# Kernel tuning notes

Measured on AMD Instinct MI355X. Metric: run time of the kernel, lower is better.

The kernel has to match this reference:

```python
import jax, jax.numpy as jnp
import numpy as np


def setup_inputs() -> dict:
    key = jax.random.key(0)
    k1, k2, k3 = jax.random.split(key, 3)
    B, K, IN, OUT = 4096, 8, 1024, 1024
    x = jax.random.normal(k1, (B, IN), dtype=jnp.float32)
    blend_weights = jax.random.uniform(k2, (B, K), dtype=jnp.float32)
    weight = jax.random.normal(k3, (K, OUT, IN), dtype=jnp.float32) * 0.01
    bias = jnp.zeros((K, OUT), dtype=jnp.float32)
    return {"x": x, "blend_weights": blend_weights, "weight": weight, "bias": bias}


def reference(x, blend_weights, weight, bias):
    # Mathematically identical to blending weights first then matvec:
    #   einsum('bk,koi->boi') then bmm  ==  per-expert GEMM then blend.
    # per-expert outputs: (b, k, o)
    expert_out = jnp.einsum('bi,koi->bko', x, weight)
    out = jnp.einsum('bk,bko->bo', blend_weights, expert_out)
    out = out + blend_weights @ bias  # (b,k) @ (k,o) -> (b,o)
    return out
```

## Files before the change

kernel.cpp:

```cpp
#include <hip/hip_runtime.h>
#include <hip/hip_bf16.h>
#include <stdint.h>

typedef short short8 __attribute__((ext_vector_type(8)));
typedef float f32x4  __attribute__((ext_vector_type(4)));
typedef unsigned short u16;

#define B_ROWS 4096
#define NEXP   8
#define IN_D   1024
#define OUT_D  1024

#define BM 128
#define BN 128
#define BK 64

__device__ __forceinline__ u16 f2bf(float f) {
    uint32_t u = __float_as_uint(f);
    uint32_t r = (u + 0x7fffu + ((u >> 16) & 1u)) >> 16;
    return (u16)r;
}

#define W_CVT_BLOCKS 8192
__global__ __launch_bounds__(256) void prep(const float* __restrict__ x,
                                            const float* __restrict__ bwt,
                                            const float* __restrict__ wgt,
                                            u16* __restrict__ ab,
                                            u16* __restrict__ wb) {
    const int bid = blockIdx.x;
    if (bid < W_CVT_BLOCKS) {
        const int i = bid * 256 + threadIdx.x;
        float4 v = reinterpret_cast<const float4*>(wgt)[i];
        ushort4 o;
        o.x = f2bf(v.x); o.y = f2bf(v.y); o.z = f2bf(v.z); o.w = f2bf(v.w);
        reinterpret_cast<ushort4*>(wb)[i] = o;
    } else {
        const int b = bid - W_CVT_BLOCKS;
        const int i4 = threadIdx.x;
        float4 v = reinterpret_cast<const float4*>(x)[(size_t)b * 256 + i4];
        float4 w0 = reinterpret_cast<const float4*>(bwt)[b * 2];
        float4 w1 = reinterpret_cast<const float4*>(bwt)[b * 2 + 1];
        float wk[8] = {w0.x, w0.y, w0.z, w0.w, w1.x, w1.y, w1.z, w1.w};
        #pragma unroll
        for (int k = 0; k < NEXP; ++k) {
            ushort4 o;
            o.x = f2bf(wk[k] * v.x); o.y = f2bf(wk[k] * v.y);
            o.z = f2bf(wk[k] * v.z); o.w = f2bf(wk[k] * v.w);
            reinterpret_cast<ushort4*>(ab)[((size_t)k * B_ROWS + b) * 256 + i4] = o;
        }
    }
}

__device__ __forceinline__ void glds16(const u16* g, u16* lds_base, int off_bytes) {
    auto gp = (const __attribute__((address_space(1))) void*)(uintptr_t)(g);
    auto lp = (__attribute__((address_space(3))) void*)(uintptr_t)((const char*)lds_base + off_bytes);
    __builtin_amdgcn_global_load_lds(gp, lp, 16, 0, 0);
}

__global__ __launch_bounds__(256) void moe_gemm(
    const u16* __restrict__ Ab,
    const u16* __restrict__ Wb,
    float* __restrict__ parts,
    float* __restrict__ out,
    int epb, int nz)
{
    __shared__ __align__(16) u16 As[BM * BK];
    __shared__ __align__(16) u16 Bs[BN * BK];

    const int nwg = gridDim.x;
    const int cpx = nwg >> 3;
    const int id  = blockIdx.x;
    const int swz = (id & 7) * cpx + (id >> 3);
    const int bz  = swz >> 8;
    const int rem = swz & 255;
    const int bm  = (rem >> 3) * BM;
    const int bn  = (rem & 7) * BN;

    const int tid  = threadIdx.x;
    const int lane = tid & 63, wid = tid >> 6;
    const int wm = wid >> 1, wn = wid & 1;
    const int lr = lane & 15, lg = lane >> 4;

    int st_row[4], st_col[4], st_off[4];
    #pragma unroll
    for (int r = 0; r < 4; ++r) {
        int c = r * 256 + wid * 64 + lane;
        st_row[r] = c >> 3;
        st_col[r] = (c & 7) * 8;
        st_off[r] = (r * 256 + wid * 64) * 16;
    }

    f32x4 acc[4][4];
    #pragma unroll
    for (int mi = 0; mi < 4; ++mi)
        #pragma unroll
        for (int ni = 0; ni < 4; ++ni)
            acc[mi][ni] = (f32x4){0.f, 0.f, 0.f, 0.f};

    const int nsteps = IN_D / BK;
    for (int e = 0; e < epb; ++e) {
        const int kexp = bz * epb + e;
        const u16* Ak = Ab + (size_t)kexp * B_ROWS * IN_D;
        const u16* Wk = Wb + (size_t)kexp * OUT_D * IN_D;

        for (int it = 0; it < nsteps; ++it) {
            const int i0 = it * BK;
            __syncthreads();
            #pragma unroll
            for (int r = 0; r < 4; ++r) {
                glds16(Ak + (size_t)(bm + st_row[r]) * IN_D + i0 + st_col[r], As, st_off[r]);
                glds16(Wk + (size_t)(bn + st_row[r]) * IN_D + i0 + st_col[r], Bs, st_off[r]);
            }
            __syncthreads();

            #pragma unroll
            for (int ks = 0; ks < 2; ++ks) {
                short8 a[4], b[4];
                #pragma unroll
                for (int mi = 0; mi < 4; ++mi)
                    a[mi] = *(const short8*)(As + (wm * 64 + mi * 16 + lr) * BK + ks * 32 + lg * 8);
                #pragma unroll
                for (int ni = 0; ni < 4; ++ni)
                    b[ni] = *(const short8*)(Bs + (wn * 64 + ni * 16 + lr) * BK + ks * 32 + lg * 8);
                #pragma unroll
                for (int mi = 0; mi < 4; ++mi)
                    #pragma unroll
                    for (int ni = 0; ni < 4; ++ni)
                        acc[mi][ni] = __builtin_amdgcn_mfma_f32_16x16x32_bf16(
                            a[mi], b[ni], acc[mi][ni], 0, 0, 0);
            }
        }
    }

    float* op = (bz == nz - 1) ? out : parts + (size_t)bz * B_ROWS * OUT_D;
    #pragma unroll
    for (int mi = 0; mi < 4; ++mi)
        #pragma unroll
        for (int ni = 0; ni < 4; ++ni)
            #pragma unroll
            for (int r = 0; r < 4; ++r) {
                const int grow = bm + wm * 64 + mi * 16 + lg * 4 + r;
                const int gcol = bn + wn * 64 + ni * 16 + lr;
                op[(size_t)grow * OUT_D + gcol] = acc[mi][ni][r];
            }
}

__global__ __launch_bounds__(256) void reduce_bias(
    const float* __restrict__ parts, const float* __restrict__ bwt,
    const float* __restrict__ bias, float* __restrict__ out, int np)
{
    const int i4 = blockIdx.x * 256 + threadIdx.x;
    const size_t total = (size_t)B_ROWS * OUT_D;
    const size_t base = (size_t)i4 * 4;
    if (base >= total) return;
    const int brow = (int)(base >> 10);
    const int o = (int)(base & 1023);

    float4 s = *reinterpret_cast<const float4*>(out + base);
    for (int z = 0; z < np; ++z) {
        float4 p = *reinterpret_cast<const float4*>(parts + (size_t)z * total + base);
        s.x += p.x; s.y += p.y; s.z += p.z; s.w += p.w;
    }
    #pragma unroll
    for (int k = 0; k < NEXP; ++k) {
        const float w = bwt[brow * NEXP + k];
        float4 bb = *reinterpret_cast<const float4*>(bias + k * OUT_D + o);
        s.x += w * bb.x; s.y += w * bb.y; s.z += w * bb.z; s.w += w * bb.w;
    }
    *reinterpret_cast<float4*>(out + base) = s;
}

__global__ __launch_bounds__(256) void naive_moe(
    const float* __restrict__ x, const float* __restrict__ bwt,
    const float* __restrict__ wgt, const float* __restrict__ bias,
    float* __restrict__ out)
{
    __shared__ float xs[IN_D];
    const int brow = blockIdx.x;
    const int o = blockIdx.y * 256 + threadIdx.x;
    for (int i = threadIdx.x; i < IN_D; i += 256) xs[i] = x[(size_t)brow * IN_D + i];
    __syncthreads();
    float acc = 0.f;
    for (int k = 0; k < NEXP; ++k) {
        const float* wr = wgt + ((size_t)k * OUT_D + o) * IN_D;
        float d = 0.f;
        for (int i = 0; i < IN_D; ++i) d += xs[i] * wr[i];
        acc += bwt[brow * NEXP + k] * (d + bias[k * OUT_D + o]);
    }
    out[(size_t)brow * OUT_D + o] = acc;
}

extern "C" void kernel_launch(void* const* d_in, const int* in_sizes, int n_in,
                              void* d_out, int out_size, void* d_ws, size_t ws_size,
                              hipStream_t stream) {
    const float* x    = (const float*)d_in[0];
    const float* bwt  = (const float*)d_in[1];
    const float* wgt  = (const float*)d_in[2];
    const float* bias = (const float*)d_in[3];
    float* out = (float*)d_out;

    const size_t a_bytes    = (size_t)NEXP * B_ROWS * IN_D * 2;
    const size_t w_bytes    = (size_t)NEXP * OUT_D * IN_D * 2;
    const size_t part_bytes = (size_t)B_ROWS * OUT_D * 4;

    if (ws_size < a_bytes + w_bytes) {
        naive_moe<<<dim3(B_ROWS, OUT_D / 256), 256, 0, stream>>>(x, bwt, wgt, bias, out);
        return;
    }

    int nz = 1;
    if      (ws_size >= a_bytes + w_bytes + 3 * part_bytes) nz = 4;
    else if (ws_size >= a_bytes + w_bytes + 1 * part_bytes) nz = 2;

    u16* ab = (u16*)d_ws;
    u16* wb = (u16*)((char*)d_ws + a_bytes);
    float* parts = (float*)((char*)d_ws + a_bytes + w_bytes);

    prep<<<W_CVT_BLOCKS + B_ROWS, 256, 0, stream>>>(x, bwt, wgt, ab, wb);

    moe_gemm<<<256 * nz, 256, 0, stream>>>(ab, wb, parts, out, NEXP / nz, nz);

    reduce_bias<<<(B_ROWS * OUT_D / 4 + 255) / 256, 256, 0, stream>>>(
        parts, bwt, bias, out, nz - 1);
}
```

Before: 211.6 us.

## Rewrite MoE GEMM as 256x256 8-wave pipelined kernel with swizzled LDS

```diff
diff --git a/kernel.cpp b/kernel.cpp
--- a/kernel.cpp
+++ b/kernel.cpp
@@ -10,10 +10,6 @@
 #define NEXP   8
 #define IN_D   1024
 #define OUT_D  1024
-
-#define BM 128
-#define BN 128
-#define BK 64
 
 __device__ __forceinline__ u16 f2bf(float f) {
     uint32_t u = __float_as_uint(f);
@@ -51,97 +47,137 @@
     }
 }
 
-__device__ __forceinline__ void glds16(const u16* g, u16* lds_base, int off_bytes) {
+__device__ __forceinline__ void glds16(const u16* g, u16* lds_base, uint32_t off) {
     auto gp = (const __attribute__((address_space(1))) void*)(uintptr_t)(g);
-    auto lp = (__attribute__((address_space(3))) void*)(uintptr_t)((const char*)lds_base + off_bytes);
+    auto lp = (__attribute__((address_space(3))) void*)(uintptr_t)((const char*)lds_base + off);
     __builtin_amdgcn_global_load_lds(gp, lp, 16, 0, 0);
 }
 
-__global__ __launch_bounds__(256) void moe_gemm(
+#define PHASE(BUF, QM, QN, LOADA, STAGE_STMT)                                     \
+  {                                                                               \
+    asm volatile("s_waitcnt vmcnt(6)" ::: "memory");                              \
+    if (LOADA) {                                                                  \
+      _Pragma("unroll") for (int mi = 0; mi < 4; ++mi)                            \
+        _Pragma("unroll") for (int ks = 0; ks < 2; ++ks)                          \
+          af[mi][ks] = *(const short8*)(ldsc + (BUF)*65536 + (QM)*16384 +         \
+                                        aRowB + mi*2048 + cXor[ks]);              \
+    }                                                                             \
+    _Pragma("unroll") for (int ni = 0; ni < 2; ++ni)                              \
+      _Pragma("unroll") for (int ks = 0; ks < 2; ++ks)                            \
+        bf[ni][ks] = *(const short8*)(ldsc + (BUF)*65536 + 32768 + (QN)*16384 +   \
+                                      bRowB + ni*2048 + cXor[ks]);                \
+    STAGE_STMT;                                                                   \
+    __builtin_amdgcn_s_barrier();                                                 \
+    __builtin_amdgcn_s_setprio(1);                                                \
+    _Pragma("unroll") for (int mi = 0; mi < 4; ++mi)                              \
+      _Pragma("unroll") for (int ni = 0; ni < 2; ++ni) {                          \
+        acc[QM][QN][mi][ni] = __builtin_amdgcn_mfma_f32_16x16x32_bf16(            \
+            af[mi][0], bf[ni][0], acc[QM][QN][mi][ni], 0, 0, 0);                  \
+        acc[QM][QN][mi][ni] = __builtin_amdgcn_mfma_f32_16x16x32_bf16(            \
+            af[mi][1], bf[ni][1], acc[QM][QN][mi][ni], 0, 0, 0);                  \
+      }                                                                           \
+    __builtin_amdgcn_s_setprio(0);                                                \
+    __builtin_amdgcn_s_barrier();                                                 \
+  }
+
+__global__ __launch_bounds__(512, 2) void moe_gemm8(
     const u16* __restrict__ Ab,
     const u16* __restrict__ Wb,
     float* __restrict__ parts,
     float* __restrict__ out,
     int epb, int nz)
 {
-    __shared__ __align__(16) u16 As[BM * BK];
-    __shared__ __align__(16) u16 Bs[BN * BK];
+    __shared__ __align__(16) u16 lds[65536];
 
     const int nwg = gridDim.x;
     const int cpx = nwg >> 3;
     const int id  = blockIdx.x;
     const int swz = (id & 7) * cpx + (id >> 3);
-    const int bz  = swz >> 8;
-    const int rem = swz & 255;
-    const int bm  = (rem >> 3) * BM;
-    const int bn  = (rem & 7) * BN;
+    const int bz  = swz >> 6;
+    const int rem = swz & 63;
+    const int bm_g = (rem >> 2) * 256;
+    const int bn_g = (rem & 3) * 256;
 
     const int tid  = threadIdx.x;
     const int lane = tid & 63, wid = tid >> 6;
-    const int wm = wid >> 1, wn = wid & 1;
+    const int wm = wid >> 2, wn = wid & 3;
     const int lr = lane & 15, lg = lane >> 4;
 
-    int st_row[4], st_col[4], st_off[4];
+    const int nt   = epb << 4;
+    const int ntm1 = nt - 1;
+    const int nit  = nt >> 1;
+
+    const int row0   = wid * 8 + (lane >> 3);
+    const int colOff = ((lane & 7) ^ (lane >> 3)) * 8;
+
+    const char* ldsc = (const char*)lds;
+    const int aRowB = (wm * 64 + lr) * 128;
+    const int bRowB = (wn * 32 + lr) * 128;
+    int cXor[2];
+    cXor[0] = (lg * 16) ^ ((lr & 7) << 4);
+    cXor[1] = (64 + lg * 16) ^ ((lr & 7) << 4);
+
+    auto STAGE = [&](int t, int isB, int h, int buf) {
+        const int kexp = bz * epb + (t >> 4);
+        const int i0 = (t & 15) << 6;
+        const u16* gp = isB
+            ? Wb + ((size_t)kexp * OUT_D + bn_g + h * 128 + row0) * IN_D + i0 + colOff
+            : Ab + ((size_t)kexp * B_ROWS + bm_g + h * 128 + row0) * IN_D + i0 + colOff;
+        const uint32_t l0 = (uint32_t)((buf << 16) + (isB << 15) + (h << 14) + (wid << 10));
+        glds16(gp, lds, l0);
+        glds16(gp + (size_t)64 * IN_D, lds, l0 + 8192);
+    };
+
+    f32x4 acc[2][2][4][2];
     #pragma unroll
-    for (int r = 0; r < 4; ++r) {
-        int c = r * 256 + wid * 64 + lane;
-        st_row[r] = c >> 3;
-        st_col[r] = (c & 7) * 8;
-        st_off[r] = (r * 256 + wid * 64) * 16;
-    }
-
-    f32x4 acc[4][4];
+    for (int a = 0; a < 2; ++a)
+      #pragma unroll
+      for (int b = 0; b < 2; ++b)
+        #pragma unroll
+        for (int c = 0; c < 4; ++c)
+          #pragma unroll
+          for (int d = 0; d < 2; ++d)
+            acc[a][b][c][d] = (f32x4){0.f, 0.f, 0.f, 0.f};
+
+    short8 af[4][2], bf[2][2];
+
+    STAGE(0, 0, 0, 0);
+    STAGE(0, 1, 0, 0);
+    STAGE(0, 1, 1, 0);
+    STAGE(0, 0, 1, 0);
+    STAGE(1, 0, 0, 1);
+    STAGE(1, 1, 0, 1);
+    asm volatile("s_waitcnt vmcnt(0)" ::: "memory");
+    __builtin_amdgcn_s_barrier();
+
+    for (int m = 0; m < nit; ++m) {
+        const int t1 = 2 * m + 1;
+        const int t2 = (t1 + 1) & ntm1;
+        const int t3 = (t1 + 2) & ntm1;
+        PHASE(0, 0, 0, 1, STAGE(t1, 1, 1, 1));
+        PHASE(0, 0, 1, 0, STAGE(t1, 0, 1, 1));
+        PHASE(0, 1, 0, 1, STAGE(t2, 0, 0, 0));
+        PHASE(0, 1, 1, 0, STAGE(t2, 1, 0, 0));
+        PHASE(1, 0, 0, 1, STAGE(t2, 1, 1, 0));
+        PHASE(1, 0, 1, 0, STAGE(t2, 0, 1, 0));
+        PHASE(1, 1, 0, 1, STAGE(t3, 0, 0, 1));
+        PHASE(1, 1, 1, 0, STAGE(t3, 1, 0, 1));
+    }
+
+    float* op = (bz == nz - 1) ? out : parts + (size_t)bz * B_ROWS * OUT_D;
     #pragma unroll
-    for (int mi = 0; mi < 4; ++mi)
+    for (int qm = 0; qm < 2; ++qm)
+      #pragma unroll
+      for (int mi = 0; mi < 4; ++mi)
         #pragma unroll
-        for (int ni = 0; ni < 4; ++ni)
-            acc[mi][ni] = (f32x4){0.f, 0.f, 0.f, 0.f};
-
-    const int nsteps = IN_D / BK;
-    for (int e = 0; e < epb; ++e) {
-        const int kexp = bz * epb + e;
-        const u16* Ak = Ab + (size_t)kexp * B_ROWS * IN_D;
-        const u16* Wk = Wb + (size_t)kexp * OUT_D * IN_D;
-
-        for (int it = 0; it < nsteps; ++it) {
-            const int i0 = it * BK;
-            __syncthreads();
+        for (int qn = 0; qn < 2; ++qn)
+          #pragma unroll
+          for (int ni = 0; ni < 2; ++ni)
             #pragma unroll
             for (int r = 0; r < 4; ++r) {
-                glds16(Ak + (size_t)(bm + st_row[r]) * IN_D + i0 + st_col[r], As, st_off[r]);
-                glds16(Wk + (size_t)(bn + st_row[r]) * IN_D + i0 + st_col[r], Bs, st_off[r]);
-            }
-            __syncthreads();
-
-            #pragma unroll
-            for (int ks = 0; ks < 2; ++ks) {
-                short8 a[4], b[4];
-                #pragma unroll
-                for (int mi = 0; mi < 4; ++mi)
-                    a[mi] = *(const short8*)(As + (wm * 64 + mi * 16 + lr) * BK + ks * 32 + lg * 8);
-                #pragma unroll
-                for (int ni = 0; ni < 4; ++ni)
-                    b[ni] = *(const short8*)(Bs + (wn * 64 + ni * 16 + lr) * BK + ks * 32 + lg * 8);
-                #pragma unroll
-                for (int mi = 0; mi < 4; ++mi)
-                    #pragma unroll
-                    for (int ni = 0; ni < 4; ++ni)
-                        acc[mi][ni] = __builtin_amdgcn_mfma_f32_16x16x32_bf16(
-                            a[mi], b[ni], acc[mi][ni], 0, 0, 0);
-            }
-        }
-    }
-
-    float* op = (bz == nz - 1) ? out : parts + (size_t)bz * B_ROWS * OUT_D;
-    #pragma unroll
-    for (int mi = 0; mi < 4; ++mi)
-        #pragma unroll
-        for (int ni = 0; ni < 4; ++ni)
-            #pragma unroll
-            for (int r = 0; r < 4; ++r) {
-                const int grow = bm + wm * 64 + mi * 16 + lg * 4 + r;
-                const int gcol = bn + wn * 64 + ni * 16 + lr;
-                op[(size_t)grow * OUT_D + gcol] = acc[mi][ni][r];
+                const int grow = bm_g + qm * 128 + wm * 64 + mi * 16 + lg * 4 + r;
+                const int gcol = bn_g + qn * 128 + wn * 32 + ni * 16 + lr;
+                op[(size_t)grow * OUT_D + gcol] = acc[qm][qn][mi][ni][r];
             }
 }
 
@@ -218,7 +254,7 @@
 
     prep<<<W_CVT_BLOCKS + B_ROWS, 256, 0, stream>>>(x, bwt, wgt, ab, wb);
 
-    moe_gemm<<<256 * nz, 256, 0, stream>>>(ab, wb, parts, out, NEXP / nz, nz);
+    moe_gemm8<<<64 * nz, 512, 0, stream>>>(ab, wb, parts, out, NEXP / nz, nz);
 
     reduce_bias<<<(B_ROWS * OUT_D / 4 + 255) / 256, 256, 0, stream>>>(
         parts, bwt, bias, out, nz - 1);
```

New measurement: 184.6 us. 1.15x faster.
